# Kernel tuning notes

Measured on AMD Instinct MI355X. Metric: run time of the kernel, lower is better.

The kernel has to match this reference:

```python
import jax, jax.numpy as jnp
import numpy as np

B, S, D, H = 4, 2048, 1024, 16
DK = D // H  # 64


def setup_inputs() -> dict:
    key = jax.random.key(0)
    ks = jax.random.split(key, 11)
    scale = 1.0 / np.sqrt(D)
    inp = {
        "query": jax.random.normal(ks[0], (B, S, D), jnp.float32),
        "key": jax.random.normal(ks[1], (B, S, D), jnp.float32),
        "value": jax.random.normal(ks[2], (B, S, D), jnp.float32),
        "Wq": jax.random.normal(ks[3], (D, D), jnp.float32) * scale,
        "bq": jnp.zeros((D,), jnp.float32),
        "Wk": jax.random.normal(ks[4], (D, D), jnp.float32) * scale,
        "bk": jnp.zeros((D,), jnp.float32),
        "Wv": jax.random.normal(ks[5], (D, D), jnp.float32) * scale,
        "bv": jnp.zeros((D,), jnp.float32),
        "Wo": jax.random.normal(ks[6], (D, D), jnp.float32) * scale,
        "bo": jnp.zeros((D,), jnp.float32),
    }
    return inp


def reference(query, key, value, Wq, bq, Wk, bk, Wv, bv, Wo, bo):
    # Projections: torch Linear computes x @ W.T + b; here W is stored as (in, out)
    def split_heads(x):
        return x.reshape(B, S, H, DK).transpose(0, 2, 1, 3)  # [B,H,S,DK]

    Q = split_heads(query @ Wq + bq)
    K = split_heads(key @ Wk + bk)
    V = split_heads(value @ Wv + bv)

    scores = jnp.einsum("bhqd,bhkd->bhqk", Q, K) / jnp.sqrt(jnp.float32(DK))
    attn = jax.nn.softmax(scores, axis=-1)  # [B,H,S,S]
    ctx = jnp.einsum("bhqk,bhkd->bhqd", attn, V)
    ctx = ctx.transpose(0, 2, 1, 3).reshape(B, S, D)
    return ctx @ Wo + bo
```

## Files before the change

### kernel.cpp

```cpp
#include <hip/hip_runtime.h>
#include <hip/hip_bf16.h>
#include <cstdint>

#define DEV __device__ __forceinline__

typedef __bf16 bf16x8 __attribute__((ext_vector_type(8)));
typedef float f32x4 __attribute__((ext_vector_type(4)));
typedef unsigned short u16;
typedef unsigned short u16x8 __attribute__((ext_vector_type(8)));
typedef unsigned short u16x4 __attribute__((ext_vector_type(4)));

#if defined(__has_builtin) && __has_builtin(__builtin_amdgcn_exp2f)
#define EXP2F(x) __builtin_amdgcn_exp2f(x)
#else
#define EXP2F(x) exp2f(x)
#endif

static constexpr float QSCALE = 0.125f * 1.44269504088896340736f;

DEV u16 f2bf(float f) {
  uint32_t x = __builtin_bit_cast(uint32_t, f);
  x += 0x7fffu + ((x >> 16) & 1u);
  return (u16)(x >> 16);
}

DEV u16x4 pack4(float a, float b, float c, float d) {
  union { __hip_bfloat162 h[2]; u16x4 u; } r;
  r.h[0] = __float22bfloat162_rn(make_float2(a, b));
  r.h[1] = __float22bfloat162_rn(make_float2(c, d));
  return r.u;
}

DEV u16x8 cvt8(const float* p) {
  const float4 v0 = *(const float4*)p;
  const float4 v1 = *(const float4*)(p + 4);
  union { __hip_bfloat162 h[4]; u16x8 u; } r;
  r.h[0] = __float22bfloat162_rn(make_float2(v0.x, v0.y));
  r.h[1] = __float22bfloat162_rn(make_float2(v0.z, v0.w));
  r.h[2] = __float22bfloat162_rn(make_float2(v1.x, v1.y));
  r.h[3] = __float22bfloat162_rn(make_float2(v1.z, v1.w));
  return r.u;
}

DEV f32x4 mfma16(bf16x8 a, bf16x8 b, f32x4 c) {
  return __builtin_amdgcn_mfma_f32_16x16x32_bf16(a, b, c, 0, 0, 0);
}

DEV void gll16(const void* g, const void* l) {
  __builtin_amdgcn_global_load_lds(
      (const __attribute__((address_space(1))) uint32_t*)g,
      (__attribute__((address_space(3))) uint32_t*)l, 16, 0, 0);
}

__global__ __launch_bounds__(256) void cvt_kernel(
    const float* __restrict__ X0, const float* __restrict__ X1,
    const float* __restrict__ X2, u16* __restrict__ Y0,
    u16* __restrict__ Y1, u16* __restrict__ Y2) {
  const float* X = (blockIdx.z == 0) ? X0 : (blockIdx.z == 1) ? X1 : X2;
  u16* Y = (blockIdx.z == 0) ? Y0 : (blockIdx.z == 1) ? Y1 : Y2;
  const size_t i = ((size_t)blockIdx.x * 256 + threadIdx.x) * 8;
  *(u16x8*)(Y + i) = cvt8(X + i);
}

__global__ __launch_bounds__(256) void wtrans_kernel(
    const float* __restrict__ W0, const float* __restrict__ W1,
    const float* __restrict__ W2, const float* __restrict__ W3,
    u16* __restrict__ T0, u16* __restrict__ T1,
    u16* __restrict__ T2, u16* __restrict__ T3) {
  const float* W = (blockIdx.z == 0) ? W0 : (blockIdx.z == 1) ? W1 : (blockIdx.z == 2) ? W2 : W3;
  u16* T = (blockIdx.z == 0) ? T0 : (blockIdx.z == 1) ? T1 : (blockIdx.z == 2) ? T2 : T3;
  __shared__ float tile[32][33];
  const int tid = threadIdx.x;
  const int r = tid >> 3, c0 = (tid & 7) * 4;
  const float4 v = *(const float4*)(W + (size_t)(blockIdx.y * 32 + r) * 1024 + blockIdx.x * 32 + c0);
  tile[r][c0 + 0] = v.x; tile[r][c0 + 1] = v.y; tile[r][c0 + 2] = v.z; tile[r][c0 + 3] = v.w;
  __syncthreads();
  u16x4 o = pack4(tile[c0 + 0][r], tile[c0 + 1][r], tile[c0 + 2][r], tile[c0 + 3][r]);
  *(u16x4*)(T + (size_t)(blockIdx.x * 32 + r) * 1024 + blockIdx.y * 32 + c0) = o;
}

template <int EPI>
__global__ __launch_bounds__(512) void gemm_kernel(
    const u16* __restrict__ X, const u16* __restrict__ Wt,
    const float* __restrict__ bias, void* __restrict__ OutV, float scale) {
  __shared__ u16 As[128 * 32];
  __shared__ u16 Bs[128 * 32];
  const int tid = threadIdx.x;
  const int w = tid >> 6, lane = tid & 63, ln = lane & 15, quad = lane >> 4;
  const int wm = w >> 1, wn = w & 1;
  const int bm = blockIdx.y * 128, bn = blockIdx.x * 128;

  f32x4 acc[2][4];
#pragma unroll
  for (int i = 0; i < 2; i++)
#pragma unroll
    for (int j = 0; j < 4; j++) acc[i][j] = f32x4{0.f, 0.f, 0.f, 0.f};

  const int lrow = w * 16 + (lane >> 2);
  const u16* ga = X + (size_t)(bm + lrow) * 1024 + (lane & 3) * 8;
  const u16* gb = Wt + (size_t)(bn + lrow) * 1024 + (lane & 3) * 8;
  const u16* lA = As + w * 512;
  const u16* lB = Bs + w * 512;

  for (int kt = 0; kt < 32; ++kt) {
    __syncthreads();
    gll16(ga + kt * 32, lA);
    gll16(gb + kt * 32, lB);
    __syncthreads();

    bf16x8 af[2], bf[4];
#pragma unroll
    for (int i = 0; i < 2; i++) af[i] = *(const bf16x8*)&As[(wm * 32 + i * 16 + ln) * 32 + quad * 8];
#pragma unroll
    for (int j = 0; j < 4; j++) bf[j] = *(const bf16x8*)&Bs[(wn * 64 + j * 16 + ln) * 32 + quad * 8];
#pragma unroll
    for (int i = 0; i < 2; i++)
#pragma unroll
      for (int j = 0; j < 4; j++) acc[i][j] = mfma16(af[i], bf[j], acc[i][j]);
  }

#pragma unroll
  for (int j = 0; j < 4; j++) {
    const int n = bn + wn * 64 + j * 16 + ln;
    const float bv = bias[n];
#pragma unroll
    for (int i = 0; i < 2; i++) {
      const int m0 = bm + wm * 32 + i * 16 + quad * 4;
      if (EPI == 0) {
        u16* O = (u16*)OutV;
        const int h = n >> 6, dk = n & 63;
#pragma unroll
        for (int r = 0; r < 4; r++) {
          const int m = m0 + r, b = m >> 11, s = m & 2047;
          O[((size_t)(b * 16 + h) * 2048 + s) * 64 + dk] = f2bf((acc[i][j][r] + bv) * scale);
        }
      } else if (EPI == 2) {
        u16* O = (u16*)OutV;
        const int b = m0 >> 11, s0 = m0 & 2047, h = n >> 6, dk = n & 63;
        u16x4 pk = pack4((acc[i][j][0] + bv) * scale, (acc[i][j][1] + bv) * scale,
                         (acc[i][j][2] + bv) * scale, (acc[i][j][3] + bv) * scale);
        *(u16x4*)(O + (size_t)((b * 16 + h) * 64 + dk) * 2048 + s0) = pk;
      } else {
        float* O = (float*)OutV;
#pragma unroll
        for (int r = 0; r < 4; r++) O[(size_t)(m0 + r) * 1024 + n] = acc[i][j][r] + bv;
      }
    }
  }
}

__global__ __launch_bounds__(256) void fattn_kernel(
    const u16* __restrict__ Q, const u16* __restrict__ K,
    const u16* __restrict__ V, u16* __restrict__ ctx) {
  __shared__ u16 Ks[64 * 72];
  __shared__ u16 Vs[64 * 72];
  __shared__ u16 Ps[4 * 32 * 72];

  const int tid = threadIdx.x;
  const int w = tid >> 6, lane = tid & 63, ln = lane & 15, quad = lane >> 4;
  const int qt = blockIdx.x, bh = blockIdx.y;
  const size_t base = (size_t)bh * 2048 * 64;

  const int sr0 = tid >> 3, sc = (tid & 7) * 8;
  const int sr1 = 32 + sr0;

  bf16x8 qf[2][2];
#pragma unroll
  for (int j = 0; j < 2; j++)
#pragma unroll
    for (int ks = 0; ks < 2; ks++)
      qf[j][ks] = *(const bf16x8*)(Q + base + (size_t)(qt * 128 + w * 32 + j * 16 + ln) * 64 + ks * 32 + quad * 8);

  float l_i[2] = {0.f, 0.f};
  f32x4 accO[4][2];
#pragma unroll
  for (int d = 0; d < 4; d++)
#pragma unroll
    for (int j = 0; j < 2; j++) accO[d][j] = f32x4{0.f, 0.f, 0.f, 0.f};

  u16x8 kr0, kr1, vr0, vr1;
  kr0 = *(const u16x8*)(K + base + (size_t)sr0 * 64 + sc);
  kr1 = *(const u16x8*)(K + base + (size_t)sr1 * 64 + sc);
  vr0 = *(const u16x8*)(V + base + (size_t)sr0 * 2048 + sc);
  vr1 = *(const u16x8*)(V + base + (size_t)sr1 * 2048 + sc);

  for (int t = 0; t < 32; ++t) {
    __syncthreads();
    *(u16x8*)&Ks[sr0 * 72 + sc] = kr0;
    *(u16x8*)&Ks[sr1 * 72 + sc] = kr1;
    *(u16x8*)&Vs[sr0 * 72 + sc] = vr0;
    *(u16x8*)&Vs[sr1 * 72 + sc] = vr1;
    __syncthreads();

    if (t < 31) {
      const int tn = t + 1;
      kr0 = *(const u16x8*)(K + base + (size_t)(tn * 64 + sr0) * 64 + sc);
      kr1 = *(const u16x8*)(K + base + (size_t)(tn * 64 + sr1) * 64 + sc);
      vr0 = *(const u16x8*)(V + base + (size_t)sr0 * 2048 + tn * 64 + sc);
      vr1 = *(const u16x8*)(V + base + (size_t)sr1 * 2048 + tn * 64 + sc);
    }

    f32x4 s[4][2];
#pragma unroll
    for (int i = 0; i < 4; i++)
#pragma unroll
      for (int j = 0; j < 2; j++) s[i][j] = f32x4{0.f, 0.f, 0.f, 0.f};
#pragma unroll
    for (int i = 0; i < 4; i++) {
#pragma unroll
      for (int ks = 0; ks < 2; ks++) {
        const bf16x8 kf = *(const bf16x8*)&Ks[(i * 16 + ln) * 72 + ks * 32 + quad * 8];
        s[i][0] = mfma16(kf, qf[0][ks], s[i][0]);
        s[i][1] = mfma16(kf, qf[1][ks], s[i][1]);
      }
    }

#pragma unroll
    for (int j = 0; j < 2; j++) {
      float sum = 0.f;
#pragma unroll
      for (int i = 0; i < 4; i++) {
#pragma unroll
        for (int r = 0; r < 4; r++) {
          const float p = EXP2F(s[i][j][r]);
          s[i][j][r] = p;
          sum += p;
        }
        *(u16x4*)&Ps[(w * 32 + j * 16 + ln) * 72 + i * 16 + quad * 4] =
            pack4(s[i][j][0], s[i][j][1], s[i][j][2], s[i][j][3]);
      }
      l_i[j] += sum;
    }

#pragma unroll
    for (int ks = 0; ks < 2; ks++) {
      const bf16x8 pf0 = *(const bf16x8*)&Ps[(w * 32 + 0 * 16 + ln) * 72 + ks * 32 + quad * 8];
      const bf16x8 pf1 = *(const bf16x8*)&Ps[(w * 32 + 1 * 16 + ln) * 72 + ks * 32 + quad * 8];
#pragma unroll
      for (int dkt = 0; dkt < 4; dkt++) {
        const bf16x8 vf = *(const bf16x8*)&Vs[(dkt * 16 + ln) * 72 + ks * 32 + quad * 8];
        accO[dkt][0] = mfma16(vf, pf0, accO[dkt][0]);
        accO[dkt][1] = mfma16(vf, pf1, accO[dkt][1]);
      }
    }
  }

  const int b = bh >> 4, h = bh & 15;
#pragma unroll
  for (int j = 0; j < 2; j++) {
    float l = l_i[j];
    l += __shfl_xor(l, 16, 64);
    l += __shfl_xor(l, 32, 64);
    const float linv = 1.0f / l;
    const int qs = qt * 128 + w * 32 + j * 16 + ln;
#pragma unroll
    for (int dkt = 0; dkt < 4; dkt++) {
      u16x4 pk = pack4(accO[dkt][j][0] * linv, accO[dkt][j][1] * linv,
                       accO[dkt][j][2] * linv, accO[dkt][j][3] * linv);
      *(u16x4*)(ctx + (size_t)(b * 2048 + qs) * 1024 + h * 64 + dkt * 16 + quad * 4) = pk;
    }
  }
}

extern "C" void kernel_launch(void* const* d_in, const int* in_sizes, int n_in,
                              void* d_out, int out_size, void* d_ws, size_t ws_size,
                              hipStream_t stream) {
  const float* q  = (const float*)d_in[0];
  const float* k  = (const float*)d_in[1];
  const float* v  = (const float*)d_in[2];
  const float* Wq = (const float*)d_in[3];
  const float* bq = (const float*)d_in[4];
  const float* Wk = (const float*)d_in[5];
  const float* bk = (const float*)d_in[6];
  const float* Wv = (const float*)d_in[7];
  const float* bv = (const float*)d_in[8];
  const float* Wo = (const float*)d_in[9];
  const float* bo = (const float*)d_in[10];

  u16* Wtq = (u16*)d_ws;
  u16* Wtk = Wtq + 1024 * 1024;
  u16* Wtv = Wtk + 1024 * 1024;
  u16* Wto = Wtv + 1024 * 1024;
  u16* qb  = Wto + 1024 * 1024;
  u16* kb  = qb + 8192 * 1024;
  u16* vb  = kb + 8192 * 1024;
  u16* Qb  = vb + 8192 * 1024;
  u16* Kb  = Qb + 8192 * 1024;
  u16* Vtb = Kb + 8192 * 1024;
  u16* Cb  = qb;

  cvt_kernel<<<dim3(4096, 1, 3), 256, 0, stream>>>(q, k, v, qb, kb, vb);
  wtrans_kernel<<<dim3(32, 32, 4), 256, 0, stream>>>(Wq, Wk, Wv, Wo, Wtq, Wtk, Wtv, Wto);

  const dim3 gg(8, 64);
  gemm_kernel<0><<<gg, 512, 0, stream>>>(qb, Wtq, bq, Qb, QSCALE);
  gemm_kernel<0><<<gg, 512, 0, stream>>>(kb, Wtk, bk, Kb, 1.0f);
  gemm_kernel<2><<<gg, 512, 0, stream>>>(vb, Wtv, bv, Vtb, 1.0f);

  fattn_kernel<<<dim3(16, 64), 256, 0, stream>>>(Qb, Kb, Vtb, Cb);

  gemm_kernel<3><<<gg, 512, 0, stream>>>(Cb, Wto, bo, d_out, 1.0f);
}
```

Measured before the change: 383.3 us.

## Double-buffer GEMM LDS loads, merge QKV projections, swap attention grid order

Result: slower. 398.6 us (+4.0%).

```diff
diff --git a/kernel.cpp b/kernel.cpp
--- a/kernel.cpp
+++ b/kernel.cpp
@@ -79,42 +79,55 @@
   *(u16x4*)(T + (size_t)(blockIdx.x * 32 + r) * 1024 + blockIdx.y * 32 + c0) = o;
 }
 
+struct GemmAcc { f32x4 a[4][4]; };
+
 template <int EPI>
-__global__ __launch_bounds__(512) void gemm_kernel(
-    const u16* __restrict__ X, const u16* __restrict__ Wt,
-    const float* __restrict__ bias, void* __restrict__ OutV, float scale) {
-  __shared__ u16 As[128 * 32];
-  __shared__ u16 Bs[128 * 32];
+DEV void gemm_core(const u16* __restrict__ X, const u16* __restrict__ Wt,
+                   const float* __restrict__ bias, void* __restrict__ OutV,
+                   float scale, u16* As0, u16* As1, u16* Bs0, u16* Bs1,
+                   int bm, int bn) {
   const int tid = threadIdx.x;
   const int w = tid >> 6, lane = tid & 63, ln = lane & 15, quad = lane >> 4;
   const int wm = w >> 1, wn = w & 1;
-  const int bm = blockIdx.y * 128, bn = blockIdx.x * 128;
-
-  f32x4 acc[2][4];
-#pragma unroll
-  for (int i = 0; i < 2; i++)
+
+  f32x4 acc[4][4];
+#pragma unroll
+  for (int i = 0; i < 4; i++)
 #pragma unroll
     for (int j = 0; j < 4; j++) acc[i][j] = f32x4{0.f, 0.f, 0.f, 0.f};
 
-  const int lrow = w * 16 + (lane >> 2);
-  const u16* ga = X + (size_t)(bm + lrow) * 1024 + (lane & 3) * 8;
-  const u16* gb = Wt + (size_t)(bn + lrow) * 1024 + (lane & 3) * 8;
-  const u16* lA = As + w * 512;
-  const u16* lB = Bs + w * 512;
+  const int srow = w * 16 + (lane >> 2);
+  const u16* ga = X + (size_t)(bm + srow) * 1024 + (lane & 3) * 8;
+  const u16* gb = Wt + (size_t)(bn + srow) * 1024 + (lane & 3) * 8;
+  const int lofs = w * 512;
+  u16* Asb[2] = {As0, As1};
+  u16* Bsb[2] = {Bs0, Bs1};
+
+  gll16(ga, Asb[0] + lofs);
+  gll16(ga + (size_t)64 * 1024, Asb[0] + 2048 + lofs);
+  gll16(gb, Bsb[0] + lofs);
+  gll16(gb + (size_t)64 * 1024, Bsb[0] + 2048 + lofs);
 
   for (int kt = 0; kt < 32; ++kt) {
+    const int cb = kt & 1;
     __syncthreads();
-    gll16(ga + kt * 32, lA);
-    gll16(gb + kt * 32, lB);
-    __syncthreads();
-
-    bf16x8 af[2], bf[4];
-#pragma unroll
-    for (int i = 0; i < 2; i++) af[i] = *(const bf16x8*)&As[(wm * 32 + i * 16 + ln) * 32 + quad * 8];
-#pragma unroll
-    for (int j = 0; j < 4; j++) bf[j] = *(const bf16x8*)&Bs[(wn * 64 + j * 16 + ln) * 32 + quad * 8];
-#pragma unroll
-    for (int i = 0; i < 2; i++)
+    if (kt < 31) {
+      const u16* ga2 = ga + (kt + 1) * 32;
+      const u16* gb2 = gb + (kt + 1) * 32;
+      gll16(ga2, Asb[cb ^ 1] + lofs);
+      gll16(ga2 + (size_t)64 * 1024, Asb[cb ^ 1] + 2048 + lofs);
+      gll16(gb2, Bsb[cb ^ 1] + lofs);
+      gll16(gb2 + (size_t)64 * 1024, Bsb[cb ^ 1] + 2048 + lofs);
+    }
+    const u16* Ac = Asb[cb];
+    const u16* Bc = Bsb[cb];
+    bf16x8 af[4], bf[4];
+#pragma unroll
+    for (int i = 0; i < 4; i++) af[i] = *(const bf16x8*)&Ac[(wm * 64 + i * 16 + ln) * 32 + quad * 8];
+#pragma unroll
+    for (int j = 0; j < 4; j++) bf[j] = *(const bf16x8*)&Bc[(wn * 64 + j * 16 + ln) * 32 + quad * 8];
+#pragma unroll
+    for (int i = 0; i < 4; i++)
 #pragma unroll
       for (int j = 0; j < 4; j++) acc[i][j] = mfma16(af[i], bf[j], acc[i][j]);
   }
@@ -124,8 +137,8 @@
     const int n = bn + wn * 64 + j * 16 + ln;
     const float bv = bias[n];
 #pragma unroll
-    for (int i = 0; i < 2; i++) {
-      const int m0 = bm + wm * 32 + i * 16 + quad * 4;
+    for (int i = 0; i < 4; i++) {
+      const int m0 = bm + wm * 64 + i * 16 + quad * 4;
       if (EPI == 0) {
         u16* O = (u16*)OutV;
         const int h = n >> 6, dk = n & 63;
@@ -149,6 +162,33 @@
   }
 }
 
+__global__ __launch_bounds__(256) void qkv_kernel(
+    const u16* __restrict__ qb, const u16* __restrict__ kb, const u16* __restrict__ vb,
+    const u16* __restrict__ Wtq, const u16* __restrict__ Wtk, const u16* __restrict__ Wtv,
+    const float* __restrict__ bq, const float* __restrict__ bk, const float* __restrict__ bv,
+    u16* __restrict__ Qb, u16* __restrict__ Kb, u16* __restrict__ Vtb) {
+  __shared__ u16 As[2][128 * 32];
+  __shared__ u16 Bs[2][128 * 32];
+  const int z = blockIdx.z;
+  const int bm = blockIdx.y * 128, bn = blockIdx.x * 128;
+  if (z == 0) {
+    gemm_core<0>(qb, Wtq, bq, Qb, QSCALE, As[0], As[1], Bs[0], Bs[1], bm, bn);
+  } else if (z == 1) {
+    gemm_core<0>(kb, Wtk, bk, Kb, 1.0f, As[0], As[1], Bs[0], Bs[1], bm, bn);
+  } else {
+    gemm_core<2>(vb, Wtv, bv, Vtb, 1.0f, As[0], As[1], Bs[0], Bs[1], bm, bn);
+  }
+}
+
+__global__ __launch_bounds__(256) void gemm_o_kernel(
+    const u16* __restrict__ X, const u16* __restrict__ Wt,
+    const float* __restrict__ bias, float* __restrict__ Out) {
+  __shared__ u16 As[2][128 * 32];
+  __shared__ u16 Bs[2][128 * 32];
+  gemm_core<3>(X, Wt, bias, Out, 1.0f, As[0], As[1], Bs[0], Bs[1],
+               blockIdx.y * 128, blockIdx.x * 128);
+}
+
 __global__ __launch_bounds__(256) void fattn_kernel(
     const u16* __restrict__ Q, const u16* __restrict__ K,
     const u16* __restrict__ V, u16* __restrict__ ctx) {
@@ -158,7 +198,7 @@
 
   const int tid = threadIdx.x;
   const int w = tid >> 6, lane = tid & 63, ln = lane & 15, quad = lane >> 4;
-  const int qt = blockIdx.x, bh = blockIdx.y;
+  const int qt = blockIdx.y, bh = blockIdx.x;
   const size_t base = (size_t)bh * 2048 * 64;
 
   const int sr0 = tid >> 3, sc = (tid & 7) * 8;
@@ -292,12 +332,10 @@
   cvt_kernel<<<dim3(4096, 1, 3), 256, 0, stream>>>(q, k, v, qb, kb, vb);
   wtrans_kernel<<<dim3(32, 32, 4), 256, 0, stream>>>(Wq, Wk, Wv, Wo, Wtq, Wtk, Wtv, Wto);
 
-  const dim3 gg(8, 64);
-  gemm_kernel<0><<<gg, 512, 0, stream>>>(qb, Wtq, bq, Qb, QSCALE);
-  gemm_kernel<0><<<gg, 512, 0, stream>>>(kb, Wtk, bk, Kb, 1.0f);
-  gemm_kernel<2><<<gg, 512, 0, stream>>>(vb, Wtv, bv, Vtb, 1.0f);
-
-  fattn_kernel<<<dim3(16, 64), 256, 0, stream>>>(Qb, Kb, Vtb, Cb);
-
-  gemm_kernel<3><<<gg, 512, 0, stream>>>(Cb, Wto, bo, d_out, 1.0f);
-}
+  qkv_kernel<<<dim3(8, 64, 3), 256, 0, stream>>>(qb, kb, vb, Wtq, Wtk, Wtv,
+                                                 bq, bk, bv, Qb, Kb, Vtb);
+
+  fattn_kernel<<<dim3(64, 16), 256, 0, stream>>>(Qb, Kb, Vtb, Cb);
+
+  gemm_o_kernel<<<dim3(8, 64), 256, 0, stream>>>(Cb, Wto, bo, (float*)d_out);
+}
```
